# Kernel tuning notes

Measured on AMD Instinct MI355X. Metric: run time of the kernel, lower is better.

## Reference

```python
import jax, jax.numpy as jnp
import numpy as np

NH, HD, MBS = 32, 64, 16   # num_heads, head_dim, mini_batch_size
BASE_LR = 1.0
ROPE_BASE = 10000.0
EPS = 1e-6


def _rotate_half(x):
    x1, x2 = jnp.split(x, 2, axis=-1)
    return jnp.concatenate((-x2, x1), axis=-1)


def _permute_qk(x):
    B, H, L, D = x.shape
    return x.reshape(B, H, L, D // 2, 2).swapaxes(-1, -2).reshape(B, H, L, D)


def _undo_permute_qk(x):
    B, H, L, D = x.shape
    return x.reshape(B, H, L, 2, D // 2).swapaxes(-1, -2).reshape(B, H, L, D)


def _ln_fwd(x, gamma, beta):
    mu = x.mean(-1, keepdims=True)
    var = x.var(-1, keepdims=True)
    return gamma * ((x - mu) / jnp.sqrt(var + EPS)) + beta


def _ln_fused_l2_bwd(x, target, gamma, beta):
    # grad of 0.5*||LN(x) - target||^2 wrt x, fused
    D = x.shape[-1]
    mu = x.mean(-1, keepdims=True)
    std = jnp.sqrt(x.var(-1, keepdims=True) + EPS)
    x_hat = (x - mu) / std
    y = gamma * x_hat + beta
    g = (y - target) * gamma
    return (D * g - g.sum(-1, keepdims=True) - x_hat * (g * x_hat).sum(-1, keepdims=True)) / (D * std)


def setup_inputs() -> dict:
    key = jax.random.key(0)
    ks = jax.random.split(key, 8)
    B, L, C, OUT = 4, 2048, 2048, 768
    s = 0.02
    return {
        "hidden_states": jax.random.normal(ks[0], (B, L, C), jnp.float32),
        "position_ids": jnp.broadcast_to(jnp.arange(L, dtype=jnp.int32)[None], (B, L)),
        "Wq": jax.random.normal(ks[1], (C, C), jnp.float32) * s,
        "Wk": jax.random.normal(ks[2], (C, C), jnp.float32) * s,
        "Wv": jax.random.normal(ks[3], (C, C), jnp.float32) * s,
        "Wo": jax.random.normal(ks[4], (C, OUT), jnp.float32) * s,
        "W1": jax.random.normal(ks[5], (NH, HD, HD), jnp.float32) * s,
        "b1": jnp.zeros((NH, 1, HD), jnp.float32),
        "ttt_lr_weight": jax.random.normal(ks[6], (NH, 1, C), jnp.float32) * s,
        "ttt_lr_bias": jnp.zeros((NH, 1), jnp.float32),
        "learnable_token_idx": jnp.zeros((MBS,), jnp.float32),
        "ttt_norm_weight": jnp.ones((NH, HD), jnp.float32),
        "ttt_norm_bias": jnp.zeros((NH, HD), jnp.float32),
        "post_norm_weight": jnp.ones((C,), jnp.float32),
        "post_norm_bias": jnp.zeros((C,), jnp.float32),
    }


def reference(hidden_states, position_ids, Wq, Wk, Wv, Wo, W1, b1,
              ttt_lr_weight, ttt_lr_bias, learnable_token_idx,
              ttt_norm_weight, ttt_norm_bias, post_norm_weight, post_norm_bias):
    B, L, C = hidden_states.shape
    NM = L // MBS
    # QKV projections -> [B, NH, L, HD]
    XQ = (hidden_states @ Wq).reshape(B, L, NH, HD).transpose(0, 2, 1, 3)
    XK = (hidden_states @ Wk).reshape(B, L, NH, HD).transpose(0, 2, 1, 3)
    XV = (hidden_states @ Wv).reshape(B, L, NH, HD).transpose(0, 2, 1, 3)
    # RoPE on positions modulo the mini-batch size
    pos = (position_ids % MBS).astype(jnp.float32)  # [B, L]
    inv_freq = 1.0 / (ROPE_BASE ** (jnp.arange(0, HD, 2, dtype=jnp.float32) / HD))
    freqs = pos[..., None] * inv_freq               # [B, L, HD/2]
    emb = jnp.concatenate((freqs, freqs), axis=-1)  # [B, L, HD]
    cos = jnp.cos(emb)[:, None]                     # [B, 1, L, HD]
    sin = jnp.sin(emb)[:, None]
    XQ, XK = _permute_qk(XQ), _permute_qk(XK)
    XQ = XQ * cos + _rotate_half(XQ) * sin
    XK = XK * cos + _rotate_half(XK) * sin
    XQ, XK = _undo_permute_qk(XQ), _undo_permute_qk(XK)
    # reshape into mini-batches: [B, NH, NM, K, HD]
    X = hidden_states.reshape(B, NM, MBS, C)
    XQ = XQ.reshape(B, NH, NM, MBS, HD)
    XK = XK.reshape(B, NH, NM, MBS, HD)
    XV = XV.reshape(B, NH, NM, MBS, HD)
    # eta: per-token learnable LR gate
    ttt_lr = jax.nn.sigmoid(
        jnp.einsum('bnkc,hdc->bhnkd', X, ttt_lr_weight)
        + ttt_lr_bias.reshape(1, NH, 1, 1, 1))              # [B,NH,NM,K,1]
    ttt_lr_eta = BASE_LR * ttt_lr.transpose(0, 1, 2, 4, 3) / HD  # [B,NH,NM,1,K]
    token_idx = jnp.clip(1.0 / jnp.arange(1, MBS + 1, dtype=jnp.float32)
                         + learnable_token_idx, 0.0, None)
    token_eta = token_idx.reshape(1, 1, 1, MBS, 1)
    eta = token_eta * ttt_lr_eta                            # [B,NH,NM,K,K]
    # TTT-Linear dual-form mini-batch scan
    ln_w = ttt_norm_weight.reshape(1, NH, 1, HD)
    ln_b = ttt_norm_bias.reshape(1, NH, 1, HD)
    W1_0 = jnp.broadcast_to(W1[None], (B, NH, HD, HD))
    b1_0 = jnp.broadcast_to(b1[None], (B, NH, 1, HD))
    tril = jnp.tril(jnp.ones((MBS, MBS), hidden_states.dtype))

    def step(carry, xs):
        W1_s, b1_s = carry
        xq, xk, xv, eta_m = xs                 # [B,NH,K,HD], eta_m [B,NH,K,K]
        Z1 = xk @ W1_s + b1_s
        target = xv - xk
        grad = _ln_fused_l2_bwd(Z1, target, ln_w, ln_b)
        Attn = tril * (xq @ xk.swapaxes(-1, -2))
        b1_bar = b1_s - (tril * eta_m) @ grad
        Z1_bar = xq @ W1_s - (eta_m * Attn) @ grad + b1_bar
        last_eta = eta_m[:, :, -1, :, None]    # [B,NH,K,1]
        W1_new = W1_s - (last_eta * xk).swapaxes(-1, -2) @ grad
        b1_new = b1_s - jnp.sum(last_eta * grad, axis=-2, keepdims=True)
        out = xq + _ln_fwd(Z1_bar, ln_w, ln_b)
        return (W1_new, b1_new), out

    xs = (XQ.transpose(2, 0, 1, 3, 4), XK.transpose(2, 0, 1, 3, 4),
          XV.transpose(2, 0, 1, 3, 4), eta.transpose(2, 0, 1, 3, 4))
    _, outs = jax.lax.scan(step, (W1_0, b1_0), xs)   # [NM,B,NH,K,HD]
    out = outs.transpose(1, 2, 0, 3, 4).reshape(B, NH, L, HD)
    out = out.transpose(0, 2, 1, 3).reshape(B, L, C)
    # post LayerNorm (eps 1e-6) and output projection
    mu = out.mean(-1, keepdims=True)
    var = out.var(-1, keepdims=True)
    out = (out - mu) / jnp.sqrt(var + EPS) * post_norm_weight + post_norm_bias
    return out @ Wo
```

## Files before the change

### kernel.cpp

```cpp
#include <hip/hip_runtime.h>
#include <cstddef>
#include <cstdint>

#define B_DIM   4
#define L_SEQ   2048
#define C_DIM   2048
#define OUT_DIM 768
#define NHEADS  32
#define HDIM    64
#define MBS_    16
#define NMINI   128
#define EPS_    1e-6f

typedef _Float16 half8 __attribute__((ext_vector_type(8)));
typedef float floatx4 __attribute__((ext_vector_type(4)));

__device__ __forceinline__ void glds16(const void* g, void* l) {
    __builtin_amdgcn_global_load_lds(
        (const __attribute__((address_space(1))) uint32_t*)g,
        (__attribute__((address_space(3))) uint32_t*)l, 16, 0, 0);
}

__device__ __forceinline__ void split8(const float4 a, const float4 b,
                                       half8& hi, half8& lo) {
    const float x[8] = {a.x, a.y, a.z, a.w, b.x, b.y, b.z, b.w};
#pragma unroll
    for (int e = 0; e < 8; e++) {
        const _Float16 h = (_Float16)x[e];
        hi[e] = h;
        lo[e] = (_Float16)(x[e] - (float)h);
    }
}

__global__ __launch_bounds__(256)
void gemm_af32(const float* __restrict__ A,
               const _Float16* __restrict__ Bhi, const _Float16* __restrict__ Blo,
               float* __restrict__ Cout, int mode, int doRope)
{
    __shared__ __align__(16) float    sA[4096];
    __shared__ __align__(16) _Float16 sBhi[4096];
    __shared__ __align__(16) _Float16 sBlo[4096];
    const int tid = threadIdx.x;
    const int m0 = blockIdx.y * 128, n0 = blockIdx.x * 128;
    const int K = 2048;

    size_t gA[4]; float* lA[4];
#pragma unroll
    for (int I = 0; I < 4; I++) {
        const int c = I * 256 + tid;
        const int row = c >> 3, seg = (c & 7) ^ (row & 7);
        gA[I] = (size_t)(m0 + row) * K + seg * 4;
        lA[I] = &sA[c * 4];
    }
    size_t gB[2]; _Float16 *lBh[2], *lBl[2];
#pragma unroll
    for (int I = 0; I < 2; I++) {
        const int c = I * 256 + tid;
        const int row = c >> 2, seg = (c & 3) ^ ((row >> 1) & 3);
        gB[I] = (size_t)(n0 + row) * K + seg * 8;
        lBh[I] = &sBhi[c * 8];
        lBl[I] = &sBlo[c * 8];
    }

    const int lane = tid & 63, quad = lane >> 4, lc = lane & 15;
    const int wv = tid >> 6, wm = wv & 1, wn = wv >> 1;
    int offA0[4], offA1[4], offB[4];
#pragma unroll
    for (int i = 0; i < 4; i++) {
        const int rA = wm * 64 + i * 16 + lc;
        offA0[i] = (rA * 8 + ((2 * quad)     ^ (rA & 7))) * 4;
        offA1[i] = (rA * 8 + ((2 * quad + 1) ^ (rA & 7))) * 4;
    }
#pragma unroll
    for (int j = 0; j < 4; j++) {
        const int rB = wn * 64 + j * 16 + lc;
        offB[j] = (rB * 4 + (quad ^ ((rB >> 1) & 3))) * 8;
    }

    floatx4 acc[4][4];
#pragma unroll
    for (int i = 0; i < 4; i++)
#pragma unroll
        for (int j = 0; j < 4; j++) acc[i][j] = (floatx4)0.0f;

    for (int k0 = 0; k0 < K; k0 += 32) {
        __syncthreads();
#pragma unroll
        for (int I = 0; I < 4; I++) glds16(A + gA[I] + k0, lA[I]);
#pragma unroll
        for (int I = 0; I < 2; I++) {
            glds16(Bhi + gB[I] + k0, lBh[I]);
            glds16(Blo + gB[I] + k0, lBl[I]);
        }
        __syncthreads();

        half8 ah[4], al[4], bh[4], bl[4];
#pragma unroll
        for (int i = 0; i < 4; i++) {
            const float4 va = *(const float4*)&sA[offA0[i]];
            const float4 vb = *(const float4*)&sA[offA1[i]];
            split8(va, vb, ah[i], al[i]);
        }
#pragma unroll
        for (int j = 0; j < 4; j++) {
            bh[j] = *(const half8*)&sBhi[offB[j]];
            bl[j] = *(const half8*)&sBlo[offB[j]];
        }
#pragma unroll
        for (int i = 0; i < 4; i++)
#pragma unroll
            for (int j = 0; j < 4; j++) {
                acc[i][j] = __builtin_amdgcn_mfma_f32_16x16x32_f16(ah[i], bh[j], acc[i][j], 0, 0, 0);
                acc[i][j] = __builtin_amdgcn_mfma_f32_16x16x32_f16(ah[i], bl[j], acc[i][j], 0, 0, 0);
                acc[i][j] = __builtin_amdgcn_mfma_f32_16x16x32_f16(al[i], bh[j], acc[i][j], 0, 0, 0);
            }
    }

    float cs[4][4], sn[4][4];
    if (doRope) {
#pragma unroll
        for (int j = 0; j < 4; j++) {
            const int ii = ((j * 16 + lc) & 63) >> 1;
            const float invf = expf(-(float)ii * 0.28782313662425574f);
#pragma unroll
            for (int r = 0; r < 4; r++) {
                const float ang = (float)(quad * 4 + r) * invf;
                sincosf(ang, &sn[j][r], &cs[j][r]);
            }
        }
    }
    const int oddcol = lc & 1;
#pragma unroll
    for (int i = 0; i < 4; i++) {
#pragma unroll
        for (int j = 0; j < 4; j++) {
            floatx4 v = acc[i][j];
            if (doRope) {
#pragma unroll
                for (int r = 0; r < 4; r++) {
                    const float partner = __shfl_xor(v[r], 1);
                    v[r] = v[r] * cs[j][r] + partner * (oddcol ? sn[j][r] : -sn[j][r]);
                }
            }
            const int n = n0 + wn * 64 + j * 16 + lc;
            if (mode == 0) {
                const int h = (n >> 6) & 31, d = n & 63;
#pragma unroll
                for (int r = 0; r < 4; r++) {
                    const int m = m0 + wm * 64 + i * 16 + quad * 4 + r;
                    const int b = m >> 11, li = m & 2047;
                    Cout[((size_t)(b * 32 + h) * 2048 + li) * 64 + d] = v[r];
                }
            } else {
#pragma unroll
                for (int r = 0; r < 4; r++) {
                    const int m = m0 + wm * 64 + i * 16 + quad * 4 + r;
                    Cout[(size_t)m * OUT_DIM + n] = v[r];
                }
            }
        }
    }
}

__global__ __launch_bounds__(256)
void wtrans_kernel(const float* __restrict__ W, _Float16* __restrict__ BThi,
                   _Float16* __restrict__ BTlo, int Nw)
{
    __shared__ float tile[32][33];
    const int t = threadIdx.x, tx = t & 31, ty = t >> 5;
    const int n0 = blockIdx.x * 32, k0 = blockIdx.y * 32;
    const int K = 2048;
#pragma unroll
    for (int r = 0; r < 4; r++)
        tile[ty + r * 8][tx] = W[(size_t)(k0 + ty + r * 8) * Nw + n0 + tx];
    __syncthreads();
#pragma unroll
    for (int r = 0; r < 4; r++) {
        const float val = tile[tx][ty + r * 8];
        const _Float16 hh = (_Float16)val;
        const size_t o = (size_t)(n0 + ty + r * 8) * K + k0 + tx;
        BThi[o] = hh;
        BTlo[o] = (_Float16)(val - (float)hh);
    }
}

__global__ __launch_bounds__(256)
void lr_kernel(const float* __restrict__ hidden, const float* __restrict__ wlr,
               const float* __restrict__ lr_bias, float* __restrict__ lrs)
{
    __shared__ float sRow[2048];
    __shared__ float sPart[32][9];
    const int m = blockIdx.x;
    const int t = threadIdx.x;
    const float* row = hidden + (size_t)m * C_DIM;
#pragma unroll
    for (int j = 0; j < 8; j++) sRow[t + j * 256] = row[t + j * 256];
    __syncthreads();
    const int h = t >> 3, p = t & 7;
    const float* w = wlr + (size_t)h * C_DIM;
    float s = 0.0f;
#pragma unroll 8
    for (int k = 0; k < 64; k++) {
        const int c = k * 32 + p * 4;
        const float4 a = *(const float4*)(sRow + c);
        const float4 b = *(const float4*)(w + c);
        s += a.x * b.x + a.y * b.y + a.z * b.z + a.w * b.w;
    }
    sPart[h][p] = s;
    __syncthreads();
    if (t < 32) {
        float v = 0.0f;
#pragma unroll
        for (int p2 = 0; p2 < 8; p2++) v += sPart[t][p2];
        v += lr_bias[t];
        const float sig = 1.0f / (1.0f + expf(-v));
        lrs[((size_t)(m >> 11) * NHEADS + t) * L_SEQ + (m & 2047)] = sig;
    }
}

__global__ __launch_bounds__(256, 1)
void scan_mfma(const float* __restrict__ XQ, const float* __restrict__ XK,
               float* __restrict__ XVo, const float* __restrict__ LRS,
               const float* __restrict__ W1i, const float* __restrict__ b1i,
               const float* __restrict__ lt, const float* __restrict__ lnw,
               const float* __restrict__ lnb)
{
    __shared__ __align__(16) float sXq[1024];
    __shared__ __align__(16) float sXk[1024];
    __shared__ __align__(16) float sXv[16 * 68];
    __shared__ __align__(16) float sW1T[4096];
    __shared__ __align__(16) float sGt[64 * 36];
    __shared__ __align__(16) float sKt[64 * 36];
    __shared__ __align__(16) float sCf[16 * 36];
    __shared__ __align__(16) float sRed[16 * 8];
    __shared__ float sMu[16], sRstd[16], sG1[16], sG2[16];
    __shared__ float sB1[64], sGam[64], sBet[64];
    __shared__ __align__(16) float sEta[32];
    __shared__ float sTok[16];

    const int bh = blockIdx.x, h = bh & 31;
    const int t = threadIdx.x;
    const int lane = t & 63, q = lane >> 4, lc = lane & 15;
    const int w = t >> 6;
    const int col = w * 16 + lc;
    const int iRow = t >> 4;
    const int c0 = (t & 15) * 4;
    const int cellP = (t & 15) ^ (iRow & 15);

    if (t < 64) { sB1[t] = b1i[h * 64 + t]; sGam[t] = lnw[h * 64 + t]; sBet[t] = lnb[h * 64 + t]; }
    if (t < 16) sTok[t] = fmaxf(1.0f / (float)(t + 1) + lt[t], 0.0f);
    if (t < 32) sEta[t] = 0.0f;
    for (int idx = t; idx < 1024; idx += 256) {
        const int r = idx >> 4, c = 16 + (idx & 15);
        sGt[r * 36 + c] = 0.0f;
        sKt[r * 36 + c] = 0.0f;
    }
    { const int r = t >> 4, c = 16 + (t & 15); sCf[r * 36 + c] = 0.0f; }

    float w1s[4][4];
#pragma unroll
    for (int t4 = 0; t4 < 4; t4++)
#pragma unroll
        for (int r = 0; r < 4; r++)
            w1s[t4][r] = W1i[h * 4096 + (16 * t4 + lc) * 64 + (16 * w + 4 * q + r)];
#pragma unroll
    for (int t4 = 0; t4 < 4; t4++)
#pragma unroll
        for (int r = 0; r < 4; r++) {
            const int nn = 16 * w + 4 * q + r, k = 16 * t4 + lc;
            sW1T[nn * 64 + ((((k >> 2) ^ (nn & 15)) << 2) | (k & 3))] = w1s[t4][r];
        }
    __syncthreads();

    const float tok15 = sTok[15];
    const float gamC = sGam[col], betC = sBet[col];
    float tokR[4];
#pragma unroll
    for (int r = 0; r < 4; r++) tokR[r] = sTok[4 * q + r];

    const size_t base = (size_t)bh * L_SEQ * HDIM;
    const float* xq_g = XQ + base;
    const float* xk_g = XK + base;
    float* xv_g = XVo + base;
    const float* lr_g = LRS + (size_t)bh * L_SEQ;

    float4 cq = *(const float4*)(xq_g + t * 4);
    float4 ck = *(const float4*)(xk_g + t * 4);
    float4 cv = *(const float4*)(xv_g + t * 4);
    float clr = lr_g[t & 15];

    for (int n = 0; n < NMINI; n++) {
        *(float4*)&sXq[iRow * 64 + (cellP << 2)] = cq;
        *(float4*)&sXk[iRow * 64 + (cellP << 2)] = ck;
        *(float4*)&sXv[iRow * 68 + c0] = cv;
        if (t < 16) sEta[t] = clr * (1.0f / 64.0f);
        const int np = (n + 1) & (NMINI - 1);
        const float4 nq = *(const float4*)(xq_g + np * 1024 + t * 4);
        const float4 nk = *(const float4*)(xk_g + np * 1024 + t * 4);
        const float4 nv = *(const float4*)(xv_g + np * 1024 + t * 4);
        const float nlr = lr_g[np * 16 + (t & 15)];
        __syncthreads();

        {
            const float le = tok15 * sEta[iRow];
            sKt[(c0 + 0) * 36 + iRow] = ck.x * le;
            sKt[(c0 + 1) * 36 + iRow] = ck.y * le;
            sKt[(c0 + 2) * 36 + iRow] = ck.z * le;
            sKt[(c0 + 3) * 36 + iRow] = ck.w * le;
        }

        half8 qh[2], ql[2], kh[2], kl[2], wh[2], wl[2];
#pragma unroll
        for (int f = 0; f < 2; f++) {
            const int ca = (8 * f + 2 * q) ^ lc, cb = (8 * f + 2 * q + 1) ^ lc;
            {
                const float4 u0 = *(const float4*)&sXq[lc * 64 + ca * 4];
                const float4 u1 = *(const float4*)&sXq[lc * 64 + cb * 4];
                split8(u0, u1, qh[f], ql[f]);
            }
            {
                const float4 u0 = *(const float4*)&sXk[lc * 64 + ca * 4];
                const float4 u1 = *(const float4*)&sXk[lc * 64 + cb * 4];
                split8(u0, u1, kh[f], kl[f]);
            }
            {
                const int rw = 16 * w + lc;
                const float4 u0 = *(const float4*)&sW1T[rw * 64 + ca * 4];
                const float4 u1 = *(const float4*)&sW1T[rw * 64 + cb * 4];
                split8(u0, u1, wh[f], wl[f]);
            }
        }

        floatx4 z1a = (floatx4)0.0f, zba = (floatx4)0.0f, at = (floatx4)0.0f;
#pragma unroll
        for (int f = 0; f < 2; f++) {
            z1a = __builtin_amdgcn_mfma_f32_16x16x32_f16(kh[f], wh[f], z1a, 0, 0, 0);
            z1a = __builtin_amdgcn_mfma_f32_16x16x32_f16(kh[f], wl[f], z1a, 0, 0, 0);
            z1a = __builtin_amdgcn_mfma_f32_16x16x32_f16(kl[f], wh[f], z1a, 0, 0, 0);
            zba = __builtin_amdgcn_mfma_f32_16x16x32_f16(qh[f], wh[f], zba, 0, 0, 0);
            zba = __builtin_amdgcn_mfma_f32_16x16x32_f16(qh[f], wl[f], zba, 0, 0, 0);
            zba = __builtin_amdgcn_mfma_f32_16x16x32_f16(ql[f], wh[f], zba, 0, 0, 0);
        }
        if (w == 0) {
#pragma unroll
            for (int f = 0; f < 2; f++) {
                at = __builtin_amdgcn_mfma_f32_16x16x32_f16(qh[f], kh[f], at, 0, 0, 0);
                at = __builtin_amdgcn_mfma_f32_16x16x32_f16(qh[f], kl[f], at, 0, 0, 0);
                at = __builtin_amdgcn_mfma_f32_16x16x32_f16(ql[f], kh[f], at, 0, 0, 0);
            }
        }

        const float b1c = sB1[col];
        float z[4], s1[4], s2[4];
#pragma unroll
        for (int r = 0; r < 4; r++) { z[r] = z1a[r] + b1c; s1[r] = z[r]; s2[r] = z[r] * z[r]; }
#pragma unroll
        for (int o = 1; o < 16; o <<= 1)
#pragma unroll
            for (int r = 0; r < 4; r++) { s1[r] += __shfl_xor(s1[r], o); s2[r] += __shfl_xor(s2[r], o); }
        if (lc == 0)
#pragma unroll
            for (int r = 0; r < 4; r++) {
                const int row = 4 * q + r;
                sRed[row * 8 + w] = s1[r];
                sRed[row * 8 + 4 + w] = s2[r];
            }
        __syncthreads();
        if (t < 16) {
            const float4 a = *(const float4*)&sRed[t * 8];
            const float4 b = *(const float4*)&sRed[t * 8 + 4];
            const float mu = (a.x + a.y + a.z + a.w) * (1.0f / 64.0f);
            const float ex2 = (b.x + b.y + b.z + b.w) * (1.0f / 64.0f);
            sMu[t] = mu;
            sRstd[t] = rsqrtf(ex2 - mu * mu + EPS_);
        }
        __syncthreads();

        float gg[4], xh[4];
#pragma unroll
        for (int r = 0; r < 4; r++) {
            const int row = 4 * q + r;
            const float mu = sMu[row], rs = sRstd[row];
            xh[r] = (z[r] - mu) * rs;
            const float xkv = sXk[row * 64 + (((((col >> 2) ^ row) & 15) << 2) | (col & 3))];
            const float tgt = sXv[row * 68 + col] - xkv;
            gg[r] = (gamC * xh[r] + betC - tgt) * gamC;
            s1[r] = gg[r]; s2[r] = gg[r] * xh[r];
        }
#pragma unroll
        for (int o = 1; o < 16; o <<= 1)
#pragma unroll
            for (int r = 0; r < 4; r++) { s1[r] += __shfl_xor(s1[r], o); s2[r] += __shfl_xor(s2[r], o); }
        if (lc == 0)
#pragma unroll
            for (int r = 0; r < 4; r++) {
                const int row = 4 * q + r;
                sRed[row * 8 + w] = s1[r];
                sRed[row * 8 + 4 + w] = s2[r];
            }
        __syncthreads();
        if (t < 16) {
            const float4 a = *(const float4*)&sRed[t * 8];
            const float4 b = *(const float4*)&sRed[t * 8 + 4];
            sG1[t] = a.x + a.y + a.z + a.w;
            sG2[t] = b.x + b.y + b.z + b.w;
        }
        __syncthreads();
#pragma unroll
        for (int r = 0; r < 4; r++) {
            const int row = 4 * q + r;
            const float rs = sRstd[row];
            const float gr = (64.0f * gg[r] - sG1[row] - xh[r] * sG2[row]) * rs * (1.0f / 64.0f);
            sGt[col * 36 + row] = gr;
        }
        if (w == 0) {
            const float ej = sEta[lc];
#pragma unroll
            for (int r = 0; r < 4; r++) {
                const int i = 4 * q + r;
                const float cf = (lc <= i) ? -tokR[r] * ej * (at[r] + 1.0f) : 0.0f;
                sCf[i * 36 + lc] = cf;
            }
        }
        __syncthreads();

        half8 cfh, cfl, gth, gtl;
        {
            const float4 u0 = *(const float4*)&sCf[lc * 36 + 8 * q];
            const float4 u1 = *(const float4*)&sCf[lc * 36 + 8 * q + 4];
            split8(u0, u1, cfh, cfl);
        }
        {
            const int rw = 16 * w + lc;
            const float4 u0 = *(const float4*)&sGt[rw * 36 + 8 * q];
            const float4 u1 = *(const float4*)&sGt[rw * 36 + 8 * q + 4];
            split8(u0, u1, gth, gtl);
        }
        zba = __builtin_amdgcn_mfma_f32_16x16x32_f16(cfh, gth, zba, 0, 0, 0);
        zba = __builtin_amdgcn_mfma_f32_16x16x32_f16(cfh, gtl, zba, 0, 0, 0);
        zba = __builtin_amdgcn_mfma_f32_16x16x32_f16(cfl, gth, zba, 0, 0, 0);
#pragma unroll
        for (int t4 = 0; t4 < 4; t4++) {
            half8 kth, ktl;
            const float4 u0 = *(const float4*)&sKt[(16 * t4 + lc) * 36 + 8 * q];
            const float4 u1 = *(const float4*)&sKt[(16 * t4 + lc) * 36 + 8 * q + 4];
            split8(u0, u1, kth, ktl);
            floatx4 up = (floatx4)0.0f;
            up = __builtin_amdgcn_mfma_f32_16x16x32_f16(gth, kth, up, 0, 0, 0);
            up = __builtin_amdgcn_mfma_f32_16x16x32_f16(gth, ktl, up, 0, 0, 0);
            up = __builtin_amdgcn_mfma_f32_16x16x32_f16(gtl, kth, up, 0, 0, 0);
#pragma unroll
            for (int r = 0; r < 4; r++) w1s[t4][r] -= up[r];
        }

        float z2[4];
#pragma unroll
        for (int r = 0; r < 4; r++) { z2[r] = zba[r] + b1c; s1[r] = z2[r]; s2[r] = z2[r] * z2[r]; }
#pragma unroll
        for (int o = 1; o < 16; o <<= 1)
#pragma unroll
            for (int r = 0; r < 4; r++) { s1[r] += __shfl_xor(s1[r], o); s2[r] += __shfl_xor(s2[r], o); }
        if (lc == 0)
#pragma unroll
            for (int r = 0; r < 4; r++) {
                const int row = 4 * q + r;
                sRed[row * 8 + w] = s1[r];
                sRed[row * 8 + 4 + w] = s2[r];
            }
        __syncthreads();
        if (t < 16) {
            const float4 a = *(const float4*)&sRed[t * 8];
            const float4 b = *(const float4*)&sRed[t * 8 + 4];
            const float mu = (a.x + a.y + a.z + a.w) * (1.0f / 64.0f);
            const float ex2 = (b.x + b.y + b.z + b.w) * (1.0f / 64.0f);
            sMu[t] = mu;
            sRstd[t] = rsqrtf(ex2 - mu * mu + EPS_);
        }
        __syncthreads();

#pragma unroll
        for (int r = 0; r < 4; r++) {
            const int row = 4 * q + r;
            const float mu = sMu[row], rs = sRstd[row];
            const float xqv = sXq[row * 64 + (((((col >> 2) ^ row) & 15) << 2) | (col & 3))];
            xv_g[n * 1024 + row * 64 + col] = xqv + gamC * ((z2[r] - mu) * rs) + betC;
        }

        {
            const float4 e0 = *(const float4*)&sEta[8 * q];
            const float4 e1 = *(const float4*)&sEta[8 * q + 4];
            const float ev[8] = {e0.x, e0.y, e0.z, e0.w, e1.x, e1.y, e1.z, e1.w};
            float p = 0.0f;
#pragma unroll
            for (int jj = 0; jj < 8; jj++)
                p += ((float)gth[jj] + (float)gtl[jj]) * ev[jj];
            p += __shfl_xor(p, 16);
            if (q == 0) sB1[col] -= tok15 * p;
        }

#pragma unroll
        for (int t4 = 0; t4 < 4; t4++)
#pragma unroll
            for (int r = 0; r < 4; r++) {
                const int nn = 16 * w + 4 * q + r, k = 16 * t4 + lc;
                sW1T[nn * 64 + ((((k >> 2) ^ (nn & 15)) << 2) | (k & 3))] = w1s[t4][r];
            }
        __syncthreads();
        cq = nq; ck = nk; cv = nv; clr = nlr;
    }
}

__global__ __launch_bounds__(256)
void postln_kernel(const float* __restrict__ Ob, const float* __restrict__ pnw,
                   const float* __restrict__ pnb, float* __restrict__ XN)
{
    const int m = blockIdx.x;
    const int b = m >> 11, l = m & 2047;
    const int t = threadIdx.x;
    float v[8];
    float s1 = 0.0f, s2 = 0.0f;
    const float* bas = Ob + (size_t)b * NHEADS * L_SEQ * HDIM + (size_t)l * HDIM;
#pragma unroll
    for (int j = 0; j < 8; j++) {
        const int c = t + j * 256;
        const int hh = c >> 6, d = c & 63;
        const float x = bas[(size_t)hh * (L_SEQ * HDIM) + d];
        v[j] = x; s1 += x; s2 += x * x;
    }
#pragma unroll
    for (int o = 1; o < 64; o <<= 1) { s1 += __shfl_xor(s1, o); s2 += __shfl_xor(s2, o); }
    __shared__ float r1[4], r2[4];
    const int w = t >> 6;
    if ((t & 63) == 0) { r1[w] = s1; r2[w] = s2; }
    __syncthreads();
    s1 = r1[0] + r1[1] + r1[2] + r1[3];
    s2 = r2[0] + r2[1] + r2[2] + r2[3];
    const float mu = s1 * (1.0f / 2048.0f);
    const float var = s2 * (1.0f / 2048.0f) - mu * mu;
    const float rstd = rsqrtf(var + EPS_);
    float* o = XN + (size_t)m * C_DIM;
#pragma unroll
    for (int j = 0; j < 8; j++) {
        const int c = t + j * 256;
        o[c] = (v[j] - mu) * rstd * pnw[c] + pnb[c];
    }
}

extern "C" void kernel_launch(void* const* d_in, const int* in_sizes, int n_in,
                              void* d_out, int out_size, void* d_ws, size_t ws_size,
                              hipStream_t stream)
{
    (void)in_sizes; (void)n_in; (void)out_size;
    const float* hidden  = (const float*)d_in[0];
    const float* Wq      = (const float*)d_in[2];
    const float* Wk      = (const float*)d_in[3];
    const float* Wv      = (const float*)d_in[4];
    const float* Wo      = (const float*)d_in[5];
    const float* W1      = (const float*)d_in[6];
    const float* b1      = (const float*)d_in[7];
    const float* wlr     = (const float*)d_in[8];
    const float* lr_bias = (const float*)d_in[9];
    const float* lt      = (const float*)d_in[10];
    const float* lnw     = (const float*)d_in[11];
    const float* lnb     = (const float*)d_in[12];
    const float* pnw     = (const float*)d_in[13];
    const float* pnb     = (const float*)d_in[14];

    const size_t TEN = (size_t)B_DIM * NHEADS * L_SEQ * HDIM;
    float* XQ  = (float*)d_ws;
    float* XK  = XQ + TEN;
    float* XVo = XK + TEN;
    float* LRS = XVo + TEN;
    const dim3 blk(256);

    _Float16* BThi = (_Float16*)d_out;
    _Float16* BTlo = BThi + (size_t)C_DIM * C_DIM;

    lr_kernel<<<dim3(B_DIM * L_SEQ), blk, 0, stream>>>(hidden, wlr, lr_bias, LRS);

    const float* Wmats[3] = {Wq, Wk, Wv};
    float* outs[3] = {XQ, XK, XVo};
    for (int p = 0; p < 3; p++) {
        wtrans_kernel<<<dim3(64, 64), blk, 0, stream>>>(Wmats[p], BThi, BTlo, C_DIM);
        gemm_af32<<<dim3(16, 64), blk, 0, stream>>>(hidden, BThi, BTlo,
                                                    outs[p], 0, (p < 2) ? 1 : 0);
    }
    scan_mfma<<<dim3(B_DIM * NHEADS), blk, 0, stream>>>(XQ, XK, XVo, LRS,
                                                        W1, b1, lt, lnw, lnb);
    float* XN = XQ;
    _Float16* WThi = (_Float16*)XK;
    _Float16* WTlo = WThi + (size_t)OUT_DIM * C_DIM;
    postln_kernel<<<dim3(B_DIM * L_SEQ), blk, 0, stream>>>(XVo, pnw, pnb, XN);
    wtrans_kernel<<<dim3(24, 64), blk, 0, stream>>>(Wo, WThi, WTlo, OUT_DIM);
    gemm_af32<<<dim3(6, 64), blk, 0, stream>>>(XN, WThi, WTlo,
                                               (float*)d_out, 1, 0);
}
```

Measured before the change: 1.474 ms.

## Rewrite TTT scan as single-wave kernel with async double-buffered LDS loads

The sequential mini-batch scan goes from four waves per block to a single 64-lane wave that owns all four 16-column tiles of W1. This removes every __syncthreads and the shared-memory reductions for the LayerNorm statistics; row sums now use only in-wave shuffles. Next-chunk XQ/XK/XV are prefetched with global_load_lds into double-buffered LDS. The trade-off is four times more MFMA and register work per wave, with 128 single-wave blocks leaving most of the GPU idle.

```diff
diff --git a/kernel.cpp b/kernel.cpp
--- a/kernel.cpp
+++ b/kernel.cpp
@@ -31,6 +31,11 @@
         lo[e] = (_Float16)(x[e] - (float)h);
     }
 }
+
+#define MFMA3(ACC, AH, AL, BH, BL)                                             \
+    ACC = __builtin_amdgcn_mfma_f32_16x16x32_f16((AH), (BH), ACC, 0, 0, 0);    \
+    ACC = __builtin_amdgcn_mfma_f32_16x16x32_f16((AH), (BL), ACC, 0, 0, 0);    \
+    ACC = __builtin_amdgcn_mfma_f32_16x16x32_f16((AL), (BH), ACC, 0, 0, 0);
 
 __global__ __launch_bounds__(256)
 void gemm_af32(const float* __restrict__ A,
@@ -110,9 +115,7 @@
         for (int i = 0; i < 4; i++)
 #pragma unroll
             for (int j = 0; j < 4; j++) {
-                acc[i][j] = __builtin_amdgcn_mfma_f32_16x16x32_f16(ah[i], bh[j], acc[i][j], 0, 0, 0);
-                acc[i][j] = __builtin_amdgcn_mfma_f32_16x16x32_f16(ah[i], bl[j], acc[i][j], 0, 0, 0);
-                acc[i][j] = __builtin_amdgcn_mfma_f32_16x16x32_f16(al[i], bh[j], acc[i][j], 0, 0, 0);
+                MFMA3(acc[i][j], ah[i], al[i], bh[j], bl[j]);
             }
     }
 
@@ -218,65 +221,75 @@
     }
 }
 
-__global__ __launch_bounds__(256, 1)
-void scan_mfma(const float* __restrict__ XQ, const float* __restrict__ XK,
-               float* __restrict__ XVo, const float* __restrict__ LRS,
-               const float* __restrict__ W1i, const float* __restrict__ b1i,
-               const float* __restrict__ lt, const float* __restrict__ lnw,
-               const float* __restrict__ lnb)
+__global__ __launch_bounds__(64, 1)
+void scan_1wave(const float* __restrict__ XQ, const float* __restrict__ XK,
+                float* __restrict__ XVo, const float* __restrict__ LRS,
+                const float* __restrict__ W1i, const float* __restrict__ b1i,
+                const float* __restrict__ lt, const float* __restrict__ lnw,
+                const float* __restrict__ lnb)
 {
-    __shared__ __align__(16) float sXq[1024];
-    __shared__ __align__(16) float sXk[1024];
-    __shared__ __align__(16) float sXv[16 * 68];
+    __shared__ __align__(16) float sXq[2][1024];
+    __shared__ __align__(16) float sXk[2][1024];
+    __shared__ __align__(16) float sXv[2][1024];
     __shared__ __align__(16) float sW1T[4096];
     __shared__ __align__(16) float sGt[64 * 36];
     __shared__ __align__(16) float sKt[64 * 36];
     __shared__ __align__(16) float sCf[16 * 36];
-    __shared__ __align__(16) float sRed[16 * 8];
-    __shared__ float sMu[16], sRstd[16], sG1[16], sG2[16];
-    __shared__ float sB1[64], sGam[64], sBet[64];
+    __shared__ __align__(16) float sB1[64];
     __shared__ __align__(16) float sEta[32];
-    __shared__ float sTok[16];
-
+
+    const int t = threadIdx.x;
+    const int q = t >> 4, lc = t & 15;
     const int bh = blockIdx.x, h = bh & 31;
-    const int t = threadIdx.x;
-    const int lane = t & 63, q = lane >> 4, lc = lane & 15;
-    const int w = t >> 6;
-    const int col = w * 16 + lc;
-    const int iRow = t >> 4;
-    const int c0 = (t & 15) * 4;
-    const int cellP = (t & 15) ^ (iRow & 15);
-
-    if (t < 64) { sB1[t] = b1i[h * 64 + t]; sGam[t] = lnw[h * 64 + t]; sBet[t] = lnb[h * 64 + t]; }
-    if (t < 16) sTok[t] = fmaxf(1.0f / (float)(t + 1) + lt[t], 0.0f);
+
+    int srcOff[4];
+#pragma unroll
+    for (int I = 0; I < 4; I++) {
+        const int c = I * 64 + t;
+        const int row = c >> 4, seg = (c & 15) ^ (row & 15);
+        srcOff[I] = row * 64 + seg * 4;
+    }
+
+    float tokR[4];
+#pragma unroll
+    for (int r = 0; r < 4; r++)
+        tokR[r] = fmaxf(1.0f / (float)(4 * q + r + 1) + lt[4 * q + r], 0.0f);
+    const float tok15 = fmaxf(1.0f / 16.0f + lt[15], 0.0f);
+    float gamR[4], betR[4];
+#pragma unroll
+    for (int j = 0; j < 4; j++) {
+        gamR[j] = lnw[h * 64 + 16 * j + lc];
+        betR[j] = lnb[h * 64 + 16 * j + lc];
+    }
+    sB1[t] = b1i[h * 64 + t];
     if (t < 32) sEta[t] = 0.0f;
-    for (int idx = t; idx < 1024; idx += 256) {
-        const int r = idx >> 4, c = 16 + (idx & 15);
+    for (int z = t; z < 1024; z += 64) {
+        const int r = z >> 4, c = 16 + (z & 15);
         sGt[r * 36 + c] = 0.0f;
         sKt[r * 36 + c] = 0.0f;
     }
-    { const int r = t >> 4, c = 16 + (t & 15); sCf[r * 36 + c] = 0.0f; }
-
-    float w1s[4][4];
-#pragma unroll
-    for (int t4 = 0; t4 < 4; t4++)
-#pragma unroll
-        for (int r = 0; r < 4; r++)
-            w1s[t4][r] = W1i[h * 4096 + (16 * t4 + lc) * 64 + (16 * w + 4 * q + r)];
-#pragma unroll
-    for (int t4 = 0; t4 < 4; t4++)
-#pragma unroll
-        for (int r = 0; r < 4; r++) {
-            const int nn = 16 * w + 4 * q + r, k = 16 * t4 + lc;
-            sW1T[nn * 64 + ((((k >> 2) ^ (nn & 15)) << 2) | (k & 3))] = w1s[t4][r];
-        }
-    __syncthreads();
-
-    const float tok15 = sTok[15];
-    const float gamC = sGam[col], betC = sBet[col];
-    float tokR[4];
-#pragma unroll
-    for (int r = 0; r < 4; r++) tokR[r] = sTok[4 * q + r];
+    for (int z = t; z < 256; z += 64) {
+        const int r = z >> 4, c = 16 + (z & 15);
+        sCf[r * 36 + c] = 0.0f;
+    }
+
+    float w1s[4][4][4];
+#pragma unroll
+    for (int w = 0; w < 4; w++)
+#pragma unroll
+        for (int t4 = 0; t4 < 4; t4++)
+#pragma unroll
+            for (int r = 0; r < 4; r++)
+                w1s[w][t4][r] = W1i[h * 4096 + (16 * t4 + lc) * 64 + (16 * w + 4 * q + r)];
+#pragma unroll
+    for (int w = 0; w < 4; w++)
+#pragma unroll
+        for (int t4 = 0; t4 < 4; t4++)
+#pragma unroll
+            for (int r = 0; r < 4; r++) {
+                const int nn = 16 * w + 4 * q + r, k = 16 * t4 + lc;
+                sW1T[nn * 64 + ((((k >> 2) ^ (nn & 15)) << 2) | (k & 3))] = w1s[w][t4][r];
+            }
 
     const size_t base = (size_t)bh * L_SEQ * HDIM;
     const float* xq_g = XQ + base;
@@ -284,229 +297,226 @@
     float* xv_g = XVo + base;
     const float* lr_g = LRS + (size_t)bh * L_SEQ;
 
-    float4 cq = *(const float4*)(xq_g + t * 4);
-    float4 ck = *(const float4*)(xk_g + t * 4);
-    float4 cv = *(const float4*)(xv_g + t * 4);
-    float clr = lr_g[t & 15];
+#pragma unroll
+    for (int I = 0; I < 4; I++) {
+        glds16(xq_g + srcOff[I], &sXq[0][(I * 64 + t) * 4]);
+        glds16(xk_g + srcOff[I], &sXk[0][(I * 64 + t) * 4]);
+        glds16(xv_g + srcOff[I], &sXv[0][(I * 64 + t) * 4]);
+    }
+    float clr = lr_g[lc];
 
     for (int n = 0; n < NMINI; n++) {
-        *(float4*)&sXq[iRow * 64 + (cellP << 2)] = cq;
-        *(float4*)&sXk[iRow * 64 + (cellP << 2)] = ck;
-        *(float4*)&sXv[iRow * 68 + c0] = cv;
+        const int buf = n & 1, nb = buf ^ 1;
+        __asm volatile("s_waitcnt vmcnt(0)" ::: "memory");
+
         if (t < 16) sEta[t] = clr * (1.0f / 64.0f);
         const int np = (n + 1) & (NMINI - 1);
-        const float4 nq = *(const float4*)(xq_g + np * 1024 + t * 4);
-        const float4 nk = *(const float4*)(xk_g + np * 1024 + t * 4);
-        const float4 nv = *(const float4*)(xv_g + np * 1024 + t * 4);
-        const float nlr = lr_g[np * 16 + (t & 15)];
-        __syncthreads();
-
-        {
-            const float le = tok15 * sEta[iRow];
-            sKt[(c0 + 0) * 36 + iRow] = ck.x * le;
-            sKt[(c0 + 1) * 36 + iRow] = ck.y * le;
-            sKt[(c0 + 2) * 36 + iRow] = ck.z * le;
-            sKt[(c0 + 3) * 36 + iRow] = ck.w * le;
-        }
-
-        half8 qh[2], ql[2], kh[2], kl[2], wh[2], wl[2];
+        const size_t go = (size_t)np * 1024;
+#pragma unroll
+        for (int I = 0; I < 4; I++) {
+            glds16(xq_g + go + srcOff[I], &sXq[nb][(I * 64 + t) * 4]);
+            glds16(xk_g + go + srcOff[I], &sXk[nb][(I * 64 + t) * 4]);
+            glds16(xv_g + go + srcOff[I], &sXv[nb][(I * 64 + t) * 4]);
+        }
+        const float nlr = lr_g[np * 16 + lc];
+        __asm volatile("s_waitcnt lgkmcnt(0)" ::: "memory");
+
+        float b1R[4];
+#pragma unroll
+        for (int j = 0; j < 4; j++) b1R[j] = sB1[16 * j + lc];
+        const float etaLc = sEta[lc];
+        const float leC = tok15 * etaLc;
+
+#pragma unroll
+        for (int i4 = 0; i4 < 4; i4++) {
+            const int phys = q + 4 * i4;
+            const float4 v = *(const float4*)&sXk[buf][lc * 64 + phys * 4];
+            const int cb = 4 * (phys ^ lc);
+            sKt[(cb + 0) * 36 + lc] = v.x * leC;
+            sKt[(cb + 1) * 36 + lc] = v.y * leC;
+            sKt[(cb + 2) * 36 + lc] = v.z * leC;
+            sKt[(cb + 3) * 36 + lc] = v.w * leC;
+        }
+
+        half8 qh[2], ql[2], kh[2], kl[2];
 #pragma unroll
         for (int f = 0; f < 2; f++) {
             const int ca = (8 * f + 2 * q) ^ lc, cb = (8 * f + 2 * q + 1) ^ lc;
             {
-                const float4 u0 = *(const float4*)&sXq[lc * 64 + ca * 4];
-                const float4 u1 = *(const float4*)&sXq[lc * 64 + cb * 4];
+                const float4 u0 = *(const float4*)&sXq[buf][lc * 64 + ca * 4];
+                const float4 u1 = *(const float4*)&sXq[buf][lc * 64 + cb * 4];
                 split8(u0, u1, qh[f], ql[f]);
             }
             {
-                const float4 u0 = *(const float4*)&sXk[lc * 64 + ca * 4];
-                const float4 u1 = *(const float4*)&sXk[lc * 64 + cb * 4];
+                const float4 u0 = *(const float4*)&sXk[buf][lc * 64 + ca * 4];
+                const float4 u1 = *(const float4*)&sXk[buf][lc * 64 + cb * 4];
                 split8(u0, u1, kh[f], kl[f]);
             }
-            {
-                const int rw = 16 * w + lc;
+        }
+
+        floatx4 at = (floatx4)0.0f;
+#pragma unroll
+        for (int f = 0; f < 2; f++) { MFMA3(at, qh[f], ql[f], kh[f], kl[f]); }
+
+        floatx4 z1a[4], zba[4];
+#pragma unroll
+        for (int j = 0; j < 4; j++) {
+            z1a[j] = (floatx4)0.0f; zba[j] = (floatx4)0.0f;
+#pragma unroll
+            for (int f = 0; f < 2; f++) {
+                const int ca = (8 * f + 2 * q) ^ lc, cb = (8 * f + 2 * q + 1) ^ lc;
+                const int rw = 16 * j + lc;
+                half8 wh, wl;
                 const float4 u0 = *(const float4*)&sW1T[rw * 64 + ca * 4];
                 const float4 u1 = *(const float4*)&sW1T[rw * 64 + cb * 4];
-                split8(u0, u1, wh[f], wl[f]);
-            }
-        }
-
-        floatx4 z1a = (floatx4)0.0f, zba = (floatx4)0.0f, at = (floatx4)0.0f;
-#pragma unroll
-        for (int f = 0; f < 2; f++) {
-            z1a = __builtin_amdgcn_mfma_f32_16x16x32_f16(kh[f], wh[f], z1a, 0, 0, 0);
-            z1a = __builtin_amdgcn_mfma_f32_16x16x32_f16(kh[f], wl[f], z1a, 0, 0, 0);
-            z1a = __builtin_amdgcn_mfma_f32_16x16x32_f16(kl[f], wh[f], z1a, 0, 0, 0);
-            zba = __builtin_amdgcn_mfma_f32_16x16x32_f16(qh[f], wh[f], zba, 0, 0, 0);
-            zba = __builtin_amdgcn_mfma_f32_16x16x32_f16(qh[f], wl[f], zba, 0, 0, 0);
-            zba = __builtin_amdgcn_mfma_f32_16x16x32_f16(ql[f], wh[f], zba, 0, 0, 0);
-        }
-        if (w == 0) {
-#pragma unroll
-            for (int f = 0; f < 2; f++) {
-                at = __builtin_amdgcn_mfma_f32_16x16x32_f16(qh[f], kh[f], at, 0, 0, 0);
-                at = __builtin_amdgcn_mfma_f32_16x16x32_f16(qh[f], kl[f], at, 0, 0, 0);
-                at = __builtin_amdgcn_mfma_f32_16x16x32_f16(ql[f], kh[f], at, 0, 0, 0);
-            }
-        }
-
-        const float b1c = sB1[col];
-        float z[4], s1[4], s2[4];
-#pragma unroll
-        for (int r = 0; r < 4; r++) { z[r] = z1a[r] + b1c; s1[r] = z[r]; s2[r] = z[r] * z[r]; }
+                split8(u0, u1, wh, wl);
+                MFMA3(z1a[j], kh[f], kl[f], wh, wl);
+                MFMA3(zba[j], qh[f], ql[f], wh, wl);
+            }
+        }
+
+        float zz[4][4], s1[4], s2[4];
+#pragma unroll
+        for (int r = 0; r < 4; r++) { s1[r] = 0.0f; s2[r] = 0.0f; }
+#pragma unroll
+        for (int j = 0; j < 4; j++)
+#pragma unroll
+            for (int r = 0; r < 4; r++) {
+                zz[j][r] = z1a[j][r] + b1R[j];
+                s1[r] += zz[j][r];
+                s2[r] += zz[j][r] * zz[j][r];
+            }
 #pragma unroll
         for (int o = 1; o < 16; o <<= 1)
 #pragma unroll
             for (int r = 0; r < 4; r++) { s1[r] += __shfl_xor(s1[r], o); s2[r] += __shfl_xor(s2[r], o); }
-        if (lc == 0)
+        float mu[4], rs[4];
+#pragma unroll
+        for (int r = 0; r < 4; r++) {
+            mu[r] = s1[r] * (1.0f / 64.0f);
+            rs[r] = rsqrtf(s2[r] * (1.0f / 64.0f) - mu[r] * mu[r] + EPS_);
+        }
+
+        float gg[4][4], xh[4][4], g1[4], g2[4];
+#pragma unroll
+        for (int r = 0; r < 4; r++) { g1[r] = 0.0f; g2[r] = 0.0f; }
+#pragma unroll
+        for (int j = 0; j < 4; j++)
 #pragma unroll
             for (int r = 0; r < 4; r++) {
-                const int row = 4 * q + r;
-                sRed[row * 8 + w] = s1[r];
-                sRed[row * 8 + 4 + w] = s2[r];
-            }
-        __syncthreads();
-        if (t < 16) {
-            const float4 a = *(const float4*)&sRed[t * 8];
-            const float4 b = *(const float4*)&sRed[t * 8 + 4];
-            const float mu = (a.x + a.y + a.z + a.w) * (1.0f / 64.0f);
-            const float ex2 = (b.x + b.y + b.z + b.w) * (1.0f / 64.0f);
-            sMu[t] = mu;
-            sRstd[t] = rsqrtf(ex2 - mu * mu + EPS_);
-        }
-        __syncthreads();
-
-        float gg[4], xh[4];
+                const int row = 4 * q + r, col = 16 * j + lc;
+                const int ad = row * 64 + (((((col >> 2) ^ row) & 15) << 2) | (col & 3));
+                xh[j][r] = (zz[j][r] - mu[r]) * rs[r];
+                const float tgt = sXv[buf][ad] - sXk[buf][ad];
+                gg[j][r] = (gamR[j] * xh[j][r] + betR[j] - tgt) * gamR[j];
+                g1[r] += gg[j][r];
+                g2[r] += gg[j][r] * xh[j][r];
+            }
+#pragma unroll
+        for (int o = 1; o < 16; o <<= 1)
+#pragma unroll
+            for (int r = 0; r < 4; r++) { g1[r] += __shfl_xor(g1[r], o); g2[r] += __shfl_xor(g2[r], o); }
+#pragma unroll
+        for (int j = 0; j < 4; j++) {
+            float4 g4;
+#pragma unroll
+            for (int r = 0; r < 4; r++) {
+                const float gr = (64.0f * gg[j][r] - g1[r] - xh[j][r] * g2[r]) * rs[r] * (1.0f / 64.0f);
+                ((float*)&g4)[r] = gr;
+            }
+            *(float4*)&sGt[(16 * j + lc) * 36 + 4 * q] = g4;
+        }
 #pragma unroll
         for (int r = 0; r < 4; r++) {
-            const int row = 4 * q + r;
-            const float mu = sMu[row], rs = sRstd[row];
-            xh[r] = (z[r] - mu) * rs;
-            const float xkv = sXk[row * 64 + (((((col >> 2) ^ row) & 15) << 2) | (col & 3))];
-            const float tgt = sXv[row * 68 + col] - xkv;
-            gg[r] = (gamC * xh[r] + betC - tgt) * gamC;
-            s1[r] = gg[r]; s2[r] = gg[r] * xh[r];
-        }
-#pragma unroll
-        for (int o = 1; o < 16; o <<= 1)
-#pragma unroll
-            for (int r = 0; r < 4; r++) { s1[r] += __shfl_xor(s1[r], o); s2[r] += __shfl_xor(s2[r], o); }
-        if (lc == 0)
-#pragma unroll
-            for (int r = 0; r < 4; r++) {
-                const int row = 4 * q + r;
-                sRed[row * 8 + w] = s1[r];
-                sRed[row * 8 + 4 + w] = s2[r];
-            }
-        __syncthreads();
-        if (t < 16) {
-            const float4 a = *(const float4*)&sRed[t * 8];
-            const float4 b = *(const float4*)&sRed[t * 8 + 4];
-            sG1[t] = a.x + a.y + a.z + a.w;
-            sG2[t] = b.x + b.y + b.z + b.w;
-        }
-        __syncthreads();
-#pragma unroll
-        for (int r = 0; r < 4; r++) {
-            const int row = 4 * q + r;
-            const float rs = sRstd[row];
-            const float gr = (64.0f * gg[r] - sG1[row] - xh[r] * sG2[row]) * rs * (1.0f / 64.0f);
-            sGt[col * 36 + row] = gr;
-        }
-        if (w == 0) {
-            const float ej = sEta[lc];
-#pragma unroll
-            for (int r = 0; r < 4; r++) {
-                const int i = 4 * q + r;
-                const float cf = (lc <= i) ? -tokR[r] * ej * (at[r] + 1.0f) : 0.0f;
-                sCf[i * 36 + lc] = cf;
-            }
-        }
-        __syncthreads();
-
-        half8 cfh, cfl, gth, gtl;
+            const int i = 4 * q + r;
+            sCf[i * 36 + lc] = (lc <= i) ? -tokR[r] * etaLc * (at[r] + 1.0f) : 0.0f;
+        }
+        __asm volatile("s_waitcnt lgkmcnt(0)" ::: "memory");
+
+        half8 cfh, cfl;
         {
             const float4 u0 = *(const float4*)&sCf[lc * 36 + 8 * q];
             const float4 u1 = *(const float4*)&sCf[lc * 36 + 8 * q + 4];
             split8(u0, u1, cfh, cfl);
         }
-        {
-            const int rw = 16 * w + lc;
-            const float4 u0 = *(const float4*)&sGt[rw * 36 + 8 * q];
-            const float4 u1 = *(const float4*)&sGt[rw * 36 + 8 * q + 4];
-            split8(u0, u1, gth, gtl);
-        }
-        zba = __builtin_amdgcn_mfma_f32_16x16x32_f16(cfh, gth, zba, 0, 0, 0);
-        zba = __builtin_amdgcn_mfma_f32_16x16x32_f16(cfh, gtl, zba, 0, 0, 0);
-        zba = __builtin_amdgcn_mfma_f32_16x16x32_f16(cfl, gth, zba, 0, 0, 0);
+        half8 gth[4], gtl[4];
+#pragma unroll
+        for (int j = 0; j < 4; j++) {
+            const float4 u0 = *(const float4*)&sGt[(16 * j + lc) * 36 + 8 * q];
+            const float4 u1 = *(const float4*)&sGt[(16 * j + lc) * 36 + 8 * q + 4];
+            split8(u0, u1, gth[j], gtl[j]);
+            MFMA3(zba[j], cfh, cfl, gth[j], gtl[j]);
+        }
 #pragma unroll
         for (int t4 = 0; t4 < 4; t4++) {
             half8 kth, ktl;
             const float4 u0 = *(const float4*)&sKt[(16 * t4 + lc) * 36 + 8 * q];
             const float4 u1 = *(const float4*)&sKt[(16 * t4 + lc) * 36 + 8 * q + 4];
             split8(u0, u1, kth, ktl);
-            floatx4 up = (floatx4)0.0f;
-            up = __builtin_amdgcn_mfma_f32_16x16x32_f16(gth, kth, up, 0, 0, 0);
-            up = __builtin_amdgcn_mfma_f32_16x16x32_f16(gth, ktl, up, 0, 0, 0);
-            up = __builtin_amdgcn_mfma_f32_16x16x32_f16(gtl, kth, up, 0, 0, 0);
-#pragma unroll
-            for (int r = 0; r < 4; r++) w1s[t4][r] -= up[r];
-        }
-
-        float z2[4];
-#pragma unroll
-        for (int r = 0; r < 4; r++) { z2[r] = zba[r] + b1c; s1[r] = z2[r]; s2[r] = z2[r] * z2[r]; }
+#pragma unroll
+            for (int w = 0; w < 4; w++) {
+                floatx4 up = (floatx4)0.0f;
+                MFMA3(up, gth[w], gtl[w], kth, ktl);
+#pragma unroll
+                for (int r = 0; r < 4; r++) w1s[w][t4][r] -= up[r];
+            }
+        }
+
+#pragma unroll
+        for (int r = 0; r < 4; r++) { s1[r] = 0.0f; s2[r] = 0.0f; }
+        float z2[4][4];
+#pragma unroll
+        for (int j = 0; j < 4; j++)
+#pragma unroll
+            for (int r = 0; r < 4; r++) {
+                z2[j][r] = zba[j][r] + b1R[j];
+                s1[r] += z2[j][r];
+                s2[r] += z2[j][r] * z2[j][r];
+            }
 #pragma unroll
         for (int o = 1; o < 16; o <<= 1)
 #pragma unroll
             for (int r = 0; r < 4; r++) { s1[r] += __shfl_xor(s1[r], o); s2[r] += __shfl_xor(s2[r], o); }
-        if (lc == 0)
+#pragma unroll
+        for (int r = 0; r < 4; r++) {
+            mu[r] = s1[r] * (1.0f / 64.0f);
+            rs[r] = rsqrtf(s2[r] * (1.0f / 64.0f) - mu[r] * mu[r] + EPS_);
+        }
+#pragma unroll
+        for (int j = 0; j < 4; j++)
 #pragma unroll
             for (int r = 0; r < 4; r++) {
-                const int row = 4 * q + r;
-                sRed[row * 8 + w] = s1[r];
-                sRed[row * 8 + 4 + w] = s2[r];
-            }
-        __syncthreads();
-        if (t < 16) {
-            const float4 a = *(const float4*)&sRed[t * 8];
-            const float4 b = *(const float4*)&sRed[t * 8 + 4];
-            const float mu = (a.x + a.y + a.z + a.w) * (1.0f / 64.0f);
-            const float ex2 = (b.x + b.y + b.z + b.w) * (1.0f / 64.0f);
-            sMu[t] = mu;
-            sRstd[t] = rsqrtf(ex2 - mu * mu + EPS_);
-        }
-        __syncthreads();
-
-#pragma unroll
-        for (int r = 0; r < 4; r++) {
-            const int row = 4 * q + r;
-            const float mu = sMu[row], rs = sRstd[row];
-            const float xqv = sXq[row * 64 + (((((col >> 2) ^ row) & 15) << 2) | (col & 3))];
-            xv_g[n * 1024 + row * 64 + col] = xqv + gamC * ((z2[r] - mu) * rs) + betC;
-        }
+                const int row = 4 * q + r, col = 16 * j + lc;
+                const int ad = row * 64 + (((((col >> 2) ^ row) & 15) << 2) | (col & 3));
+                xv_g[n * 1024 + row * 64 + col] =
+                    sXq[buf][ad] + gamR[j] * ((z2[j][r] - mu[r]) * rs[r]) + betR[j];
+            }
 
         {
             const float4 e0 = *(const float4*)&sEta[8 * q];
             const float4 e1 = *(const float4*)&sEta[8 * q + 4];
             const float ev[8] = {e0.x, e0.y, e0.z, e0.w, e1.x, e1.y, e1.z, e1.w};
-            float p = 0.0f;
-#pragma unroll
-            for (int jj = 0; jj < 8; jj++)
-                p += ((float)gth[jj] + (float)gtl[jj]) * ev[jj];
-            p += __shfl_xor(p, 16);
-            if (q == 0) sB1[col] -= tok15 * p;
-        }
-
-#pragma unroll
-        for (int t4 = 0; t4 < 4; t4++)
-#pragma unroll
-            for (int r = 0; r < 4; r++) {
-                const int nn = 16 * w + 4 * q + r, k = 16 * t4 + lc;
-                sW1T[nn * 64 + ((((k >> 2) ^ (nn & 15)) << 2) | (k & 3))] = w1s[t4][r];
-            }
-        __syncthreads();
-        cq = nq; ck = nk; cv = nv; clr = nlr;
+#pragma unroll
+            for (int w = 0; w < 4; w++) {
+                float p = 0.0f;
+#pragma unroll
+                for (int jj = 0; jj < 8; jj++)
+                    p += ((float)gth[w][jj] + (float)gtl[w][jj]) * ev[jj];
+                p += __shfl_xor(p, 16);
+                if (q == 0) sB1[16 * w + lc] -= tok15 * p;
+            }
+        }
+
+#pragma unroll
+        for (int w = 0; w < 4; w++)
+#pragma unroll
+            for (int t4 = 0; t4 < 4; t4++)
+#pragma unroll
+                for (int r = 0; r < 4; r++) {
+                    const int nn = 16 * w + 4 * q + r, k = 16 * t4 + lc;
+                    sW1T[nn * 64 + ((((k >> 2) ^ (nn & 15)) << 2) | (k & 3))] = w1s[w][t4][r];
+                }
+        clr = nlr;
     }
 }
 
@@ -550,7 +560,7 @@
                               void* d_out, int out_size, void* d_ws, size_t ws_size,
                               hipStream_t stream)
 {
-    (void)in_sizes; (void)n_in; (void)out_size;
+    (void)in_sizes; (void)n_in; (void)out_size; (void)ws_size;
     const float* hidden  = (const float*)d_in[0];
     const float* Wq      = (const float*)d_in[2];
     const float* Wk      = (const float*)d_in[3];
@@ -585,8 +595,8 @@
         gemm_af32<<<dim3(16, 64), blk, 0, stream>>>(hidden, BThi, BTlo,
                                                     outs[p], 0, (p < 2) ? 1 : 0);
     }
-    scan_mfma<<<dim3(B_DIM * NHEADS), blk, 0, stream>>>(XQ, XK, XVo, LRS,
-                                                        W1, b1, lt, lnw, lnb);
+    scan_1wave<<<dim3(B_DIM * NHEADS), dim3(64), 0, stream>>>(XQ, XK, XVo, LRS,
+                                                              W1, b1, lt, lnw, lnb);
     float* XN = XQ;
     _Float16* WThi = (_Float16*)XK;
     _Float16* WTlo = WThi + (size_t)OUT_DIM * C_DIM;
```

New measurement: 1.846 ms. 1.25x slower.
